# Optimization experiments

Measured on AMD Instinct MI355X. Metric: run time of the kernel, lower is better.

The kernel has to match this reference:

```python
import jax, jax.numpy as jnp
import numpy as np

N = 200000   # nodes
E = 600000   # edges (avg degree 3, proof graphs are sparse)
L = 4        # num_layers
ND = 64      # ndim (hardcoded in module)
ED = 12      # edim (hardcoded in module)
V = 80       # len(atom_map)
SCALE = 1.0 / np.sqrt(ND).astype(np.float32)


def setup_inputs() -> dict:
    key = jax.random.key(0)
    ks = jax.random.split(key, 20)
    nrm = lambda k, s: jax.random.normal(k, s, jnp.float32) * 0.05
    return {
        "atoms": jax.random.randint(ks[0], (N,), 0, V),
        "edge_index": jax.random.randint(ks[1], (2, E), 0, N),
        "edge_ids": jax.random.randint(ks[2], (E,), 0, 3),
        "atom_emb": nrm(ks[3], (V, ND)),
        "edge_emb": nrm(ks[4], (3, ED)),
        # dim 0: 0 = r2c convs, 1 = c2r convs; dim 1: layer
        "Wq": nrm(ks[5], (2, L, ND, ND)), "bq": nrm(ks[6], (2, L, ND)),
        "Wk": nrm(ks[7], (2, L, ND, ND)), "bk": nrm(ks[8], (2, L, ND)),
        "Wv": nrm(ks[9], (2, L, ND, ND)), "bv": nrm(ks[10], (2, L, ND)),
        "We": nrm(ks[11], (2, L, ED, ND)),            # lin_edge, bias=False (PyG)
        "Ws": nrm(ks[12], (2, L, ND, ND)), "bs": nrm(ks[13], (2, L, ND)),  # root skip
        "aggr_W": nrm(ks[14], (2 * ND, ND)), "aggr_b": nrm(ks[15], (ND,)),
    }


def tconv(x, src, tgt, e_proj, Wq, bq, Wk, bk, Wv, bv, Ws, bs):
    """PyG TransformerConv (heads=1, concat=True, root_weight=True).
    Messages flow src -> tgt; softmax grouped by tgt."""
    q = x @ Wq + bq                                   # [N, ND]
    k = x @ Wk + bk
    v = x @ Wv + bv
    ke = k[src] + e_proj                              # [E, ND]
    ve = v[src] + e_proj
    alpha = jnp.einsum('ed,ed->e', q[tgt], ke) * SCALE
    amax = jax.ops.segment_max(alpha, tgt, num_segments=N)
    ex = jnp.exp(alpha - amax[tgt])
    den = jax.ops.segment_sum(ex, tgt, num_segments=N)
    w = ex / (den[tgt] + 1e-16)                       # segment softmax
    out = jax.ops.segment_sum(ve * w[:, None], tgt, num_segments=N)
    return out + x @ Ws + bs                          # skip connection


def reference(atoms, edge_index, edge_ids, atom_emb, edge_emb,
              Wq, bq, Wk, bk, Wv, bv, We, Ws, bs, aggr_W, aggr_b):
    # dropout omitted (eval mode / identity)
    x = atom_emb[atoms]                               # [N, ND]
    e = edge_emb[edge_ids]                            # [E, ED]
    src, tgt = edge_index[0], edge_index[1]
    for hop in range(L):
        r2c = tconv(x, src, tgt, e @ We[0, hop],
                    Wq[0, hop], bq[0, hop], Wk[0, hop], bk[0, hop],
                    Wv[0, hop], bv[0, hop], Ws[0, hop], bs[0, hop])
        # edge_index.flip(0): swap src/tgt
        c2r = tconv(x, tgt, src, e @ We[1, hop],
                    Wq[1, hop], bq[1, hop], Wk[1, hop], bk[1, hop],
                    Wv[1, hop], bv[1, hop], Ws[1, hop], bs[1, hop])
        h = jnp.concatenate([r2c, c2r], axis=-1) @ aggr_W + aggr_b
        x = jax.nn.gelu(h, approximate=False)         # torch GELU = exact erf
    return x
```

## Files before the change

### kernel.cpp

```cpp
#include <hip/hip_runtime.h>
#include <hip/hip_bf16.h>

typedef unsigned short u16;
typedef unsigned int u32;
typedef unsigned long long u64;
typedef __attribute__((ext_vector_type(8))) short short8v;
typedef __attribute__((ext_vector_type(4))) float f32x4;

#define SCALE 0.125f

__device__ __forceinline__ float bf2f(u16 u){
    union { u32 i; float f; } c; c.i = ((u32)u) << 16; return c.f;
}
__device__ __forceinline__ u16 f2bf(float f){
    __hip_bfloat16 h = __float2bfloat16(f);
    union { __hip_bfloat16 h; u16 u; } c; c.h = h; return c.u;
}

__global__ void k_gather(const int* __restrict__ atoms, const float* __restrict__ emb,
                         u16* __restrict__ x, int n){
    int i = blockIdx.x * blockDim.x + threadIdx.x;
    if (i >= n * 16) return;
    int node = i >> 4, f = i & 15;
    int a = atoms[node];
    float4 v = ((const float4*)emb)[a * 16 + f];
    ushort4 o = { f2bf(v.x), f2bf(v.y), f2bf(v.z), f2bf(v.w) };
    ((ushort4*)x)[i] = o;
}

__global__ void k_ew(const float* __restrict__ edge_emb, const float* __restrict__ We,
                     float* __restrict__ EW){
    int t = blockIdx.x * blockDim.x + threadIdx.x;
    if (t >= 2 * 4 * 3 * 64) return;
    int j = t & 63, r = t >> 6;
    int eid = r % 3, dh = r / 3;
    float s = 0.f;
    for (int c = 0; c < 12; ++c)
        s += edge_emb[eid * 12 + c] * We[(dh * 12 + c) * 64 + j];
    EW[(dh * 3 + eid) * 64 + j] = s;
}

__global__ void k_count(const int* __restrict__ ei, u32* cnt_t, u32* cnt_s, int E){
    int e = blockIdx.x * blockDim.x + threadIdx.x;
    if (e >= E) return;
    atomicAdd(&cnt_t[ei[E + e]], 1u);
    atomicAdd(&cnt_s[ei[e]], 1u);
}

__global__ __launch_bounds__(256) void k_scan(
    const u32* __restrict__ cnt_t, const u32* __restrict__ cnt_s,
    u32* __restrict__ start_t, u32* __restrict__ start_s,
    u64* __restrict__ totals, int n)
{
    __shared__ u32 wsum_t[4], wsum_s[4];
    __shared__ u32 base_t, base_s;
    const int t0 = blockIdx.x * 1024 + threadIdx.x * 4;
    u32 ct[4], cs[4];
    #pragma unroll
    for (int j = 0; j < 4; ++j){
        int idx = t0 + j;
        ct[j] = (idx < n) ? cnt_t[idx] : 0u;
        cs[j] = (idx < n) ? cnt_s[idx] : 0u;
    }
    u32 tsum_t = ct[0] + ct[1] + ct[2] + ct[3];
    u32 tsum_s = cs[0] + cs[1] + cs[2] + cs[3];
    const int lane = threadIdx.x & 63, wv = threadIdx.x >> 6;
    u32 it = tsum_t, is = tsum_s;
    for (int d = 1; d < 64; d <<= 1){
        u32 a = __shfl_up(it, d);
        u32 b = __shfl_up(is, d);
        if (lane >= d){ it += a; is += b; }
    }
    if (lane == 63){ wsum_t[wv] = it; wsum_s[wv] = is; }
    __syncthreads();
    if (threadIdx.x == 0){
        u32 a0 = wsum_t[0], a1 = wsum_t[1], a2 = wsum_t[2], a3 = wsum_t[3];
        u32 b0 = wsum_s[0], b1 = wsum_s[1], b2 = wsum_s[2], b3 = wsum_s[3];
        u64 old = atomicAdd(totals, ((u64)(b0 + b1 + b2 + b3) << 32) | (u64)(a0 + a1 + a2 + a3));
        base_t = (u32)(old & 0xFFFFFFFFull);
        base_s = (u32)(old >> 32);
        wsum_t[0] = 0; wsum_t[1] = a0; wsum_t[2] = a0 + a1; wsum_t[3] = a0 + a1 + a2;
        wsum_s[0] = 0; wsum_s[1] = b0; wsum_s[2] = b0 + b1; wsum_s[3] = b0 + b1 + b2;
    }
    __syncthreads();
    u32 ex_t = base_t + wsum_t[wv] + (it - tsum_t);
    u32 ex_s = base_s + wsum_s[wv] + (is - tsum_s);
    #pragma unroll
    for (int j = 0; j < 4; ++j){
        int idx = t0 + j;
        if (idx < n){
            start_t[idx] = ex_t; start_s[idx] = ex_s;
            ex_t += ct[j]; ex_s += cs[j];
        }
    }
}

__global__ void k_fill(const int* __restrict__ ei, const int* __restrict__ eids,
                       const u32* __restrict__ start_t, const u32* __restrict__ start_s,
                       u32* cur_t, u32* cur_s, int* adj_t, int* adj_s, int E){
    int e = blockIdx.x * blockDim.x + threadIdx.x;
    if (e >= E) return;
    int s = ei[e], t = ei[E + e], id = eids[e];
    u32 p = atomicAdd(&cur_t[t], 1u);
    adj_t[start_t[t] + p] = s | (id << 20);
    u32 p2 = atomicAdd(&cur_s[s], 1u);
    adj_s[start_s[s] + p2] = t | (id << 20);
}

__global__ __launch_bounds__(256) void k_gemm4(
    const u16* __restrict__ x,
    const float* __restrict__ Wq, const float* __restrict__ bq,
    const float* __restrict__ Wk, const float* __restrict__ bk,
    const float* __restrict__ Wv, const float* __restrict__ bv,
    const float* __restrict__ Ws, const float* __restrict__ bs,
    int dh,
    u16* __restrict__ q, u16* __restrict__ k, u16* __restrict__ v,
    u16* __restrict__ outd, int n)
{
    __shared__ __align__(16) u16 Wt[4][64][64];
    __shared__ __align__(16) u16 Xh[64][64];
    const int tid = threadIdx.x;
    const int row0 = blockIdx.x * 64;

    const float* wsrc[4] = { Wq + dh * 4096, Wk + dh * 4096, Wv + dh * 4096, Ws + dh * 4096 };
    for (int m = 0; m < 4; ++m){
        for (int i = tid; i < 1024; i += 256){
            int kk = i >> 4, n4 = (i & 15) * 4;
            float4 w = ((const float4*)(wsrc[m] + (size_t)kk * 64))[i & 15];
            float wf[4] = { w.x, w.y, w.z, w.w };
            #pragma unroll
            for (int c = 0; c < 4; ++c){
                int nn = n4 + c;
                int ps = (kk >> 3) ^ (nn & 7);
                Wt[m][nn][ps * 8 + (kk & 7)] = f2bf(wf[c]);
            }
        }
    }
    for (int i = tid; i < 512; i += 256){
        int r = i >> 3, f = i & 7;
        int gr = row0 + r;
        short8v val = {0,0,0,0,0,0,0,0};
        if (gr < n) val = *(const short8v*)&x[(size_t)gr * 64 + f * 8];
        int ps = f ^ (r & 7);
        *(short8v*)&Xh[r][ps * 8] = val;
    }
    __syncthreads();

    const int wv = tid >> 6, l = tid & 63;
    const int lr = l & 15, lk = l >> 4;
    short8v ah[2];
    #pragma unroll
    for (int ks = 0; ks < 2; ++ks){
        int r = wv * 16 + lr;
        int ps = (lk + 4 * ks) ^ (r & 7);
        ah[ks] = *(const short8v*)&Xh[r][ps * 8];
    }
    const float* bsrc[4] = { bq + dh * 64, bk + dh * 64, bv + dh * 64, bs + dh * 64 };
    u16* outs[4] = { q, k, v, outd };
    for (int m = 0; m < 4; ++m){
        #pragma unroll
        for (int ct = 0; ct < 4; ++ct){
            int col = ct * 16 + lr;
            int s0 = (lk + 0) ^ (col & 7);
            int s1 = (lk + 4) ^ (col & 7);
            short8v b0 = *(const short8v*)&Wt[m][col][s0 * 8];
            short8v b1 = *(const short8v*)&Wt[m][col][s1 * 8];
            float bb = bsrc[m][col];
            f32x4 acc = { bb, bb, bb, bb };
            acc = __builtin_amdgcn_mfma_f32_16x16x32_bf16(ah[0], b0, acc, 0, 0, 0);
            acc = __builtin_amdgcn_mfma_f32_16x16x32_bf16(ah[1], b1, acc, 0, 0, 0);
            int grb = row0 + wv * 16 + lk * 4;
            u16* o = outs[m];
            #pragma unroll
            for (int j = 0; j < 4; ++j)
                if (grb + j < n) o[(size_t)(grb + j) * 64 + col] = f2bf(acc[j]);
        }
    }
}

__global__ __launch_bounds__(256) void k_attn(
    const u16* __restrict__ q, const u16* __restrict__ k, const u16* __restrict__ v,
    const int* __restrict__ adj, const u32* __restrict__ start, const u32* __restrict__ cnt,
    const float* __restrict__ EW, u16* __restrict__ outd, int n)
{
    int tid = blockIdx.x * blockDim.x + threadIdx.x;
    int node = tid >> 4;
    int l = tid & 15;
    if (node >= n) return;
    int st = (int)start[node];
    int c  = (int)cnt[node];
    ushort4 qu = ((const ushort4*)q)[node * 16 + l];
    float qx = bf2f(qu.x), qy = bf2f(qu.y), qz = bf2f(qu.z), qw = bf2f(qu.w);
    float4 acc = {0.f, 0.f, 0.f, 0.f};
    float s = 0.f;
    for (int i = 0; i < c; ++i){
        int a = adj[st + i];
        int srcn = a & 0xFFFFF;
        int eid  = ((u32)a) >> 20;
        float4 ew = ((const float4*)EW)[eid * 16 + l];
        ushort4 ku = ((const ushort4*)k)[srcn * 16 + l];
        float kx = bf2f(ku.x) + ew.x, ky = bf2f(ku.y) + ew.y;
        float kz = bf2f(ku.z) + ew.z, kw = bf2f(ku.w) + ew.w;
        float d = qx * kx + qy * ky + qz * kz + qw * kw;
        d += __shfl_xor(d, 1); d += __shfl_xor(d, 2);
        d += __shfl_xor(d, 4); d += __shfl_xor(d, 8);
        float ex = expf(d * SCALE);
        ushort4 vu = ((const ushort4*)v)[srcn * 16 + l];
        acc.x += ex * (bf2f(vu.x) + ew.x);
        acc.y += ex * (bf2f(vu.y) + ew.y);
        acc.z += ex * (bf2f(vu.z) + ew.z);
        acc.w += ex * (bf2f(vu.w) + ew.w);
        s += ex;
    }
    float inv = 1.0f / (s + 1e-16f);
    ushort4 ou = ((const ushort4*)outd)[node * 16 + l];
    ushort4 no = { f2bf(bf2f(ou.x) + acc.x * inv), f2bf(bf2f(ou.y) + acc.y * inv),
                   f2bf(bf2f(ou.z) + acc.z * inv), f2bf(bf2f(ou.w) + acc.w * inv) };
    ((ushort4*)outd)[node * 16 + l] = no;
}

__global__ __launch_bounds__(256) void k_aggr(
    const u16* __restrict__ o0, const u16* __restrict__ o1,
    const float* __restrict__ A, const float* __restrict__ b,
    u16* __restrict__ x, float* __restrict__ out_f, int write_out, int n)
{
    __shared__ __align__(16) u16 Wt[64][128];
    __shared__ __align__(16) u16 Ah[64][128];
    const int tid = threadIdx.x;
    const int row0 = blockIdx.x * 64;

    for (int i = tid; i < 2048; i += 256){
        int kk = i >> 4, n4 = (i & 15) * 4;
        float4 w = ((const float4*)(A + (size_t)kk * 64))[i & 15];
        float wf[4] = { w.x, w.y, w.z, w.w };
        #pragma unroll
        for (int c = 0; c < 4; ++c){
            int nn = n4 + c;
            int ps = (kk >> 3) ^ (nn & 7);
            Wt[nn][ps * 8 + (kk & 7)] = f2bf(wf[c]);
        }
    }
    for (int i = tid; i < 1024; i += 256){
        int r = i >> 4, j = i & 15;
        int gr = row0 + r;
        short8v val = {0,0,0,0,0,0,0,0};
        if (gr < n){
            if (j < 8) val = *(const short8v*)&o0[(size_t)gr * 64 + j * 8];
            else       val = *(const short8v*)&o1[(size_t)gr * 64 + (j - 8) * 8];
        }
        int ps = j ^ (r & 7);
        *(short8v*)&Ah[r][ps * 8] = val;
    }
    __syncthreads();

    const int wv = tid >> 6, l = tid & 63;
    const int lr = l & 15, lk = l >> 4;
    short8v ah[4];
    #pragma unroll
    for (int ks = 0; ks < 4; ++ks){
        int r = wv * 16 + lr;
        int ps = (lk + 4 * ks) ^ (r & 7);
        ah[ks] = *(const short8v*)&Ah[r][ps * 8];
    }
    #pragma unroll
    for (int ct = 0; ct < 4; ++ct){
        int col = ct * 16 + lr;
        float bb = b[col];
        f32x4 acc = { bb, bb, bb, bb };
        #pragma unroll
        for (int ks = 0; ks < 4; ++ks){
            int ps = (lk + 4 * ks) ^ (col & 7);
            short8v bf = *(const short8v*)&Wt[col][ps * 8];
            acc = __builtin_amdgcn_mfma_f32_16x16x32_bf16(ah[ks], bf, acc, 0, 0, 0);
        }
        int grb = row0 + wv * 16 + lk * 4;
        #pragma unroll
        for (int j = 0; j < 4; ++j){
            if (grb + j >= n) continue;
            float h = acc[j];
            float g = 0.5f * h * (1.0f + erff(h * 0.70710678118654752f));
            x[(size_t)(grb + j) * 64 + col] = f2bf(g);
            if (write_out) out_f[(size_t)(grb + j) * 64 + col] = g;
        }
    }
}

extern "C" void kernel_launch(void* const* d_in, const int* in_sizes, int n_in,
                              void* d_out, int out_size, void* d_ws, size_t ws_size,
                              hipStream_t stream)
{
    const int* atoms      = (const int*)d_in[0];
    const int* ei         = (const int*)d_in[1];
    const int* eids       = (const int*)d_in[2];
    const float* atom_emb = (const float*)d_in[3];
    const float* edge_emb = (const float*)d_in[4];
    const float* Wq = (const float*)d_in[5];  const float* bq = (const float*)d_in[6];
    const float* Wk = (const float*)d_in[7];  const float* bk = (const float*)d_in[8];
    const float* Wv = (const float*)d_in[9];  const float* bv = (const float*)d_in[10];
    const float* We = (const float*)d_in[11];
    const float* Ws = (const float*)d_in[12]; const float* bs = (const float*)d_in[13];
    const float* aggr_W = (const float*)d_in[14];
    const float* aggr_b = (const float*)d_in[15];

    const int N = in_sizes[0];
    const int E = in_sizes[1] / 2;

    char* p = (char*)d_ws;
    auto alloc = [&](size_t bytes){
        void* r = (void*)p;
        p += (bytes + 255) & ~(size_t)255;
        return r;
    };
    u16*   x   = (u16*)  alloc((size_t)N * 64 * 2);
    u16*   qb  = (u16*)  alloc((size_t)N * 64 * 2);
    u16*   kb  = (u16*)  alloc((size_t)N * 64 * 2);
    u16*   vb  = (u16*)  alloc((size_t)N * 64 * 2);
    u16*   o0  = (u16*)  alloc((size_t)N * 64 * 2);
    u16*   o1  = (u16*)  alloc((size_t)N * 64 * 2);
    float* EWt = (float*)alloc(2 * 4 * 3 * 64 * 4);
    int* adj_t = (int*)alloc((size_t)E * 4);
    int* adj_s = (int*)alloc((size_t)E * 4);
    u32* start_t = (u32*)alloc((size_t)N * 4);
    u32* start_s = (u32*)alloc((size_t)N * 4);
    u32* zb = (u32*)alloc(((size_t)4 * N + 2) * 4);
    u32* cnt_t = zb;
    u32* cnt_s = zb + N;
    u32* cur_t = zb + 2 * (size_t)N;
    u32* cur_s = zb + 3 * (size_t)N;
    u64* totals = (u64*)(zb + 4 * (size_t)N);

    hipMemsetAsync(zb, 0, ((size_t)4 * N + 2) * 4, stream);

    k_gather<<<(N * 16 + 255) / 256, 256, 0, stream>>>(atoms, atom_emb, x, N);
    k_ew<<<6, 256, 0, stream>>>(edge_emb, We, EWt);
    k_count<<<(E + 255) / 256, 256, 0, stream>>>(ei, cnt_t, cnt_s, E);
    k_scan<<<(N + 1023) / 1024, 256, 0, stream>>>(cnt_t, cnt_s, start_t, start_s, totals, N);
    k_fill<<<(E + 255) / 256, 256, 0, stream>>>(ei, eids, start_t, start_s, cur_t, cur_s, adj_t, adj_s, E);

    const int gB = (N + 63) / 64;
    const int gA = (N * 16 + 255) / 256;
    for (int hop = 0; hop < 4; ++hop){
        int dh0 = hop;
        int dh1 = 4 + hop;
        k_gemm4<<<gB, 256, 0, stream>>>(x, Wq, bq, Wk, bk, Wv, bv, Ws, bs, dh0, qb, kb, vb, o0, N);
        k_attn<<<gA, 256, 0, stream>>>(qb, kb, vb, adj_t, start_t, cnt_t, EWt + dh0 * 192, o0, N);
        k_gemm4<<<gB, 256, 0, stream>>>(x, Wq, bq, Wk, bk, Wv, bv, Ws, bs, dh1, qb, kb, vb, o1, N);
        k_attn<<<gA, 256, 0, stream>>>(qb, kb, vb, adj_s, start_s, cnt_s, EWt + dh1 * 192, o1, N);
        k_aggr<<<gB, 256, 0, stream>>>(o0, o1, aggr_W, aggr_b, x, (float*)d_out, hop == 3 ? 1 : 0, N);
    }
}
```

Before: 1.122 ms.

## Move root-skip projection from QKV GEMM into aggregation kernel

The skip projection x@Ws+bs for both directions is now computed inside the aggregation kernel, with the attention result added before the final aggregation GEMM. This drops the write of the skip output from the GEMM kernel and the read-modify-write of it in the attention kernel. In exchange the aggregation kernel needs more LDS, an extra GEMM stage, and a round trip through LDS for the intermediate tile. It reads x and writes x in place, which is only safe because each block reads its own rows before writing them. The attention kernel now writes its output directly.

```diff
diff --git a/kernel.cpp b/kernel.cpp
--- a/kernel.cpp
+++ b/kernel.cpp
@@ -107,23 +107,21 @@
     adj_s[start_s[s] + p2] = t | (id << 20);
 }
 
-__global__ __launch_bounds__(256) void k_gemm4(
+__global__ __launch_bounds__(256) void k_gemm3(
     const u16* __restrict__ x,
     const float* __restrict__ Wq, const float* __restrict__ bq,
     const float* __restrict__ Wk, const float* __restrict__ bk,
     const float* __restrict__ Wv, const float* __restrict__ bv,
-    const float* __restrict__ Ws, const float* __restrict__ bs,
     int dh,
-    u16* __restrict__ q, u16* __restrict__ k, u16* __restrict__ v,
-    u16* __restrict__ outd, int n)
+    u16* __restrict__ q, u16* __restrict__ k, u16* __restrict__ v, int n)
 {
-    __shared__ __align__(16) u16 Wt[4][64][64];
+    __shared__ __align__(16) u16 Wt[3][64][64];
     __shared__ __align__(16) u16 Xh[64][64];
     const int tid = threadIdx.x;
     const int row0 = blockIdx.x * 64;
 
-    const float* wsrc[4] = { Wq + dh * 4096, Wk + dh * 4096, Wv + dh * 4096, Ws + dh * 4096 };
-    for (int m = 0; m < 4; ++m){
+    const float* wsrc[3] = { Wq + dh * 4096, Wk + dh * 4096, Wv + dh * 4096 };
+    for (int m = 0; m < 3; ++m){
         for (int i = tid; i < 1024; i += 256){
             int kk = i >> 4, n4 = (i & 15) * 4;
             float4 w = ((const float4*)(wsrc[m] + (size_t)kk * 64))[i & 15];
@@ -155,9 +153,9 @@
         int ps = (lk + 4 * ks) ^ (r & 7);
         ah[ks] = *(const short8v*)&Xh[r][ps * 8];
     }
-    const float* bsrc[4] = { bq + dh * 64, bk + dh * 64, bv + dh * 64, bs + dh * 64 };
-    u16* outs[4] = { q, k, v, outd };
-    for (int m = 0; m < 4; ++m){
+    const float* bsrc[3] = { bq + dh * 64, bk + dh * 64, bv + dh * 64 };
+    u16* outs[3] = { q, k, v };
+    for (int m = 0; m < 3; ++m){
         #pragma unroll
         for (int ct = 0; ct < 4; ++ct){
             int col = ct * 16 + lr;
@@ -213,19 +211,23 @@
         s += ex;
     }
     float inv = 1.0f / (s + 1e-16f);
-    ushort4 ou = ((const ushort4*)outd)[node * 16 + l];
-    ushort4 no = { f2bf(bf2f(ou.x) + acc.x * inv), f2bf(bf2f(ou.y) + acc.y * inv),
-                   f2bf(bf2f(ou.z) + acc.z * inv), f2bf(bf2f(ou.w) + acc.w * inv) };
+    ushort4 no = { f2bf(acc.x * inv), f2bf(acc.y * inv),
+                   f2bf(acc.z * inv), f2bf(acc.w * inv) };
     ((ushort4*)outd)[node * 16 + l] = no;
 }
 
 __global__ __launch_bounds__(256) void k_aggr(
-    const u16* __restrict__ o0, const u16* __restrict__ o1,
+    const u16* __restrict__ a0, const u16* __restrict__ a1, const u16* __restrict__ xin,
+    const float* __restrict__ Ws, const float* __restrict__ bs, int hop,
     const float* __restrict__ A, const float* __restrict__ b,
-    u16* __restrict__ x, float* __restrict__ out_f, int write_out, int n)
+    u16* __restrict__ xout, float* __restrict__ out_f, int write_out, int n)
 {
-    __shared__ __align__(16) u16 Wt[64][128];
-    __shared__ __align__(16) u16 Ah[64][128];
+    __shared__ __align__(16) u16 lds[20480];
+    u16 (*Wt)[128] = (u16(*)[128])lds;
+    u16 (*Xt)[64]  = (u16(*)[64])(lds + 8192);
+    u16 (*Wst0)[64]= (u16(*)[64])(lds + 8192 + 4096);
+    u16 (*Wst1)[64]= (u16(*)[64])(lds + 8192 + 8192);
+    u16 (*Ah)[128] = (u16(*)[128])(lds + 8192);
     const int tid = threadIdx.x;
     const int row0 = blockIdx.x * 64;
 
@@ -240,21 +242,81 @@
             Wt[nn][ps * 8 + (kk & 7)] = f2bf(wf[c]);
         }
     }
-    for (int i = tid; i < 1024; i += 256){
-        int r = i >> 4, j = i & 15;
+    for (int i = tid; i < 512; i += 256){
+        int r = i >> 3, f = i & 7;
         int gr = row0 + r;
         short8v val = {0,0,0,0,0,0,0,0};
-        if (gr < n){
-            if (j < 8) val = *(const short8v*)&o0[(size_t)gr * 64 + j * 8];
-            else       val = *(const short8v*)&o1[(size_t)gr * 64 + (j - 8) * 8];
-        }
-        int ps = j ^ (r & 7);
-        *(short8v*)&Ah[r][ps * 8] = val;
+        if (gr < n) val = *(const short8v*)&xin[(size_t)gr * 64 + f * 8];
+        int ps = f ^ (r & 7);
+        *(short8v*)&Xt[r][ps * 8] = val;
+    }
+    const float* ws0 = Ws + (size_t)hop * 4096;
+    const float* ws1 = Ws + (size_t)(4 + hop) * 4096;
+    for (int i = tid; i < 1024; i += 256){
+        int kk = i >> 4, n4 = (i & 15) * 4;
+        float4 w0 = ((const float4*)(ws0 + (size_t)kk * 64))[i & 15];
+        float4 w1 = ((const float4*)(ws1 + (size_t)kk * 64))[i & 15];
+        float f0[4] = { w0.x, w0.y, w0.z, w0.w };
+        float f1[4] = { w1.x, w1.y, w1.z, w1.w };
+        #pragma unroll
+        for (int c = 0; c < 4; ++c){
+            int nn = n4 + c;
+            int ps = (kk >> 3) ^ (nn & 7);
+            Wst0[nn][ps * 8 + (kk & 7)] = f2bf(f0[c]);
+            Wst1[nn][ps * 8 + (kk & 7)] = f2bf(f1[c]);
+        }
     }
     __syncthreads();
 
     const int wv = tid >> 6, l = tid & 63;
     const int lr = l & 15, lk = l >> 4;
+    short8v xf[2];
+    #pragma unroll
+    for (int ks = 0; ks < 2; ++ks){
+        int r = wv * 16 + lr;
+        int ps = (lk + 4 * ks) ^ (r & 7);
+        xf[ks] = *(const short8v*)&Xt[r][ps * 8];
+    }
+    f32x4 S[2][4];
+    const u16* asrc[2] = { a0, a1 };
+    const int grb = row0 + wv * 16 + lk * 4;
+    #pragma unroll
+    for (int d = 0; d < 2; ++d){
+        const float* bsd = bs + (size_t)(d * 4 + hop) * 64;
+        u16 (*Wst)[64] = d ? Wst1 : Wst0;
+        #pragma unroll
+        for (int ct = 0; ct < 4; ++ct){
+            int col = ct * 16 + lr;
+            int s0 = (lk + 0) ^ (col & 7);
+            int s1 = (lk + 4) ^ (col & 7);
+            short8v b0 = *(const short8v*)&Wst[col][s0 * 8];
+            short8v b1 = *(const short8v*)&Wst[col][s1 * 8];
+            float bb = bsd[col];
+            f32x4 acc = { bb, bb, bb, bb };
+            acc = __builtin_amdgcn_mfma_f32_16x16x32_bf16(xf[0], b0, acc, 0, 0, 0);
+            acc = __builtin_amdgcn_mfma_f32_16x16x32_bf16(xf[1], b1, acc, 0, 0, 0);
+            #pragma unroll
+            for (int j = 0; j < 4; ++j)
+                if (grb + j < n) acc[j] += bf2f(asrc[d][(size_t)(grb + j) * 64 + col]);
+            S[d][ct] = acc;
+        }
+    }
+    __syncthreads();
+    #pragma unroll
+    for (int d = 0; d < 2; ++d){
+        #pragma unroll
+        for (int ct = 0; ct < 4; ++ct){
+            int col = ct * 16 + lr;
+            int kk = d * 64 + col;
+            #pragma unroll
+            for (int j = 0; j < 4; ++j){
+                int r = wv * 16 + lk * 4 + j;
+                int ps = (kk >> 3) ^ (r & 7);
+                Ah[r][ps * 8 + (kk & 7)] = f2bf(S[d][ct][j]);
+            }
+        }
+    }
+    __syncthreads();
     short8v ah[4];
     #pragma unroll
     for (int ks = 0; ks < 4; ++ks){
@@ -273,13 +335,12 @@
             short8v bf = *(const short8v*)&Wt[col][ps * 8];
             acc = __builtin_amdgcn_mfma_f32_16x16x32_bf16(ah[ks], bf, acc, 0, 0, 0);
         }
-        int grb = row0 + wv * 16 + lk * 4;
         #pragma unroll
         for (int j = 0; j < 4; ++j){
             if (grb + j >= n) continue;
             float h = acc[j];
             float g = 0.5f * h * (1.0f + erff(h * 0.70710678118654752f));
-            x[(size_t)(grb + j) * 64 + col] = f2bf(g);
+            xout[(size_t)(grb + j) * 64 + col] = f2bf(g);
             if (write_out) out_f[(size_t)(grb + j) * 64 + col] = g;
         }
     }
@@ -342,10 +403,11 @@
     for (int hop = 0; hop < 4; ++hop){
         int dh0 = hop;
         int dh1 = 4 + hop;
-        k_gemm4<<<gB, 256, 0, stream>>>(x, Wq, bq, Wk, bk, Wv, bv, Ws, bs, dh0, qb, kb, vb, o0, N);
+        k_gemm3<<<gB, 256, 0, stream>>>(x, Wq, bq, Wk, bk, Wv, bv, dh0, qb, kb, vb, N);
         k_attn<<<gA, 256, 0, stream>>>(qb, kb, vb, adj_t, start_t, cnt_t, EWt + dh0 * 192, o0, N);
-        k_gemm4<<<gB, 256, 0, stream>>>(x, Wq, bq, Wk, bk, Wv, bv, Ws, bs, dh1, qb, kb, vb, o1, N);
+        k_gemm3<<<gB, 256, 0, stream>>>(x, Wq, bq, Wk, bk, Wv, bv, dh1, qb, kb, vb, N);
         k_attn<<<gA, 256, 0, stream>>>(qb, kb, vb, adj_s, start_s, cnt_s, EWt + dh1 * 192, o1, N);
-        k_aggr<<<gB, 256, 0, stream>>>(o0, o1, aggr_W, aggr_b, x, (float*)d_out, hop == 3 ? 1 : 0, N);
-    }
-}
+        k_aggr<<<gB, 256, 0, stream>>>(o0, o1, x, Ws, bs, hop, aggr_W, aggr_b,
+                                       x, (float*)d_out, hop == 3 ? 1 : 0, N);
+    }
+}
```

Result: slower. 1.155 ms (+3.0%).
